# Performance work log

Measured on AMD Instinct MI355X. Metric: run time of the kernel, lower is better.

## Reference

```python
import jax, jax.numpy as jnp
import numpy as np

N = 10000
E = 256000
MUL = 32            # multiplicity per l (hidden_sizes = [32]*4)
NB = 10             # nbasis_funcs
RMAX = 3.5          # max_radius
NAVG = 25.6         # navg_neighbors
NGRAPH = 16         # number of graphs in batch
SLICES = [(0, 1), (1, 4), (4, 9), (9, 16)]  # l=0..3 blocks of the 16-dim SH rep


def _sph_harm(u):
    """Real spherical harmonics l=0..3, component normalization, on unit vectors. [E,16]"""
    x, y, z = u[:, 0], u[:, 1], u[:, 2]
    one = jnp.ones_like(x)
    s3 = 3.0 ** 0.5
    s15 = 15.0 ** 0.5
    s5 = 5.0 ** 0.5
    a = (35.0 / 8.0) ** 0.5
    b = 105.0 ** 0.5
    c = (21.0 / 8.0) ** 0.5
    d = 7.0 ** 0.5 / 2.0
    cols = [
        one,
        s3 * x, s3 * y, s3 * z,
        s15 * x * y, s15 * y * z, 0.5 * s5 * (3 * z * z - 1), s15 * x * z, 0.5 * s15 * (x * x - y * y),
        a * y * (3 * x * x - y * y), b * x * y * z, c * y * (5 * z * z - 1), d * z * (5 * z * z - 3),
        c * x * (5 * z * z - 1), 0.5 * b * z * (x * x - y * y), a * x * (x * x - 3 * y * y),
    ]
    return jnp.stack(cols, axis=1)


def _radial(emb, W1, W2):
    # FullyConnectedNet-style MLP with fan-in normalization and silu
    h = jax.nn.silu(emb @ W1 / (NB ** 0.5))
    return h @ W2 / (W1.shape[1] ** 0.5)


def _edge_geometry(pos, edge_src, edge_dst):
    vec = pos[edge_src] - pos[edge_dst]          # [E,3]
    r = jnp.linalg.norm(vec, axis=1)             # [E]
    u = vec / (r[:, None] + 1e-9)
    sh = _sph_harm(u)                            # [E,16]
    t = jnp.clip(r / RMAX, 0.0, 1.0)
    cutoff = jnp.where(r < RMAX, 0.5 * (jnp.cos(jnp.pi * t) + 1.0), 0.0)
    edge_attr = cutoff[:, None] * sh             # [E,16]
    centers = jnp.linspace(0.0, RMAX, NB)
    step = RMAX / (NB - 1)
    emb = jnp.exp(-(((r[:, None] - centers) / step) ** 2)) / 1.12 * (NB ** 0.5)
    return edge_attr, emb


def _layer(feat, edge_src, edge_dst, edge_attr, emb, Wsc, Wr1, Wr2):
    """Gated interaction block: self-connection + per-edge radial-weighted TP conv + gate."""
    n = feat.shape[0]
    # self-connection: per-l channel mixing
    sc = jnp.concatenate(
        [jnp.einsum('nci,co->noi', feat[:, :, a:b], Wsc[l]) for l, (a, b) in enumerate(SLICES)],
        axis=2) / (MUL ** 0.5)
    # per-edge weights from radial MLP: [E, 2 paths, 4 l's, MUL]
    w = _radial(emb, Wr1, Wr2).reshape(-1, 2, 4, MUL)
    xs = feat[edge_src]                          # [E,MUL,16] gather
    # path A (0e x Yl -> l) for l=0, plus path B (l x Yl -> 0e) for l=1..3 -> scalar slot
    scal = w[:, 0, 0, :] * xs[:, :, 0] * edge_attr[:, 0:1]
    parts = []
    for l, (a, b) in enumerate(SLICES):
        if l == 0:
            continue
        scal = scal + w[:, 1, l, :] * jnp.einsum('eci,ei->ec', xs[:, :, a:b], edge_attr[:, a:b])
        parts.append(w[:, 0, l, :, None] * xs[:, :, 0:1] * edge_attr[:, None, a:b])
    msg = jnp.concatenate([scal[:, :, None]] + parts, axis=2)   # [E,MUL,16]
    agg = jax.ops.segment_sum(msg, edge_dst, num_segments=n) / (NAVG ** 0.5)
    y = sc + agg
    # equivariant gate: silu on scalars, sigmoid(scalar) gates l>0 features
    s = y[:, :, 0]
    return jnp.concatenate(
        [jax.nn.silu(s)[:, :, None], y[:, :, 1:] * jax.nn.sigmoid(s)[:, :, None]], axis=2)


def _forward(pos, x, batch, edge_src, edge_dst, W_sc, Wr1, Wr2, Wf1, Wf2):
    n = pos.shape[0]
    edge_attr, emb = _edge_geometry(pos, edge_src, edge_dst)
    # lift scalar input features into the full l=0..3 layout
    feat = jnp.zeros((n, MUL, 16), x.dtype).at[:, :, 0].set(x)
    for i in range(3):
        feat = _layer(feat, edge_src, edge_dst, edge_attr, emb, W_sc[i], Wr1[i], Wr2[i])
    # final interaction block -> 1x0e output per node
    wf = _radial(emb, Wf1, Wf2).reshape(-1, 4, MUL)             # [E,4,MUL]
    xs = feat[edge_src]
    ms = wf[:, 0, :] * xs[:, :, 0] * edge_attr[:, 0:1]
    for l, (a, b) in enumerate(SLICES):
        if l == 0:
            continue
        ms = ms + wf[:, l, :] * jnp.einsum('eci,ei->ec', xs[:, :, a:b], edge_attr[:, a:b])
    node = jax.ops.segment_sum(ms.sum(axis=1) / (MUL ** 0.5), edge_dst, num_segments=n) / (NAVG ** 0.5)
    out = jax.ops.segment_sum(node, batch, num_segments=NGRAPH) / (NAVG ** 0.5)
    return out.flatten()


def setup_inputs() -> dict:
    key = jax.random.key(0)
    ks = jax.random.split(key, 10)
    pos = jax.random.uniform(ks[0], (N, 3), jnp.float32) * 5.0
    x = jax.random.normal(ks[1], (N, MUL), jnp.float32)
    batch = jnp.sort(jax.random.randint(ks[2], (N,), 0, NGRAPH, jnp.int32))
    edge_src = jax.random.randint(ks[3], (E,), 0, N, jnp.int32)
    edge_dst = jax.random.randint(ks[4], (E,), 0, N, jnp.int32)
    W_sc = jax.random.normal(ks[5], (3, 4, MUL, MUL), jnp.float32)
    Wr1 = jax.random.normal(ks[6], (3, NB, 64), jnp.float32)
    Wr2 = jax.random.normal(ks[7], (3, 64, 2 * 4 * MUL), jnp.float32)
    Wf1 = jax.random.normal(ks[8], (NB, 64), jnp.float32)
    Wf2 = jax.random.normal(ks[9], (64, 4 * MUL), jnp.float32)
    return {"pos": pos, "x": x, "batch": batch, "edge_src": edge_src, "edge_dst": edge_dst,
            "W_sc": W_sc, "Wr1": Wr1, "Wr2": Wr2, "Wf1": Wf1, "Wf2": Wf2}


def reference(pos, x, batch, edge_src, edge_dst, W_sc, Wr1, Wr2, Wf1, Wf2):
    return _forward(pos, x, batch, edge_src, edge_dst, W_sc, Wr1, Wr2, Wf1, Wf2)
```

## Files before the change

kernel.cpp:

```cpp
#include <hip/hip_runtime.h>
#include <math.h>

#define NN 10000
#define EE 256000
#define NGR 16
#define ECAP 150016

#define RSQRT10F   0.31622776601683794f
#define EMB_SCALE  2.8234621965789103f
#define INV_SQRT_MUL  0.17677669529663687f
#define INV_SQRT_NAVG 0.19764235376052372f
#define SCREC      (0.125f * INV_SQRT_NAVG)
#define STEPF      0.3888888888888889f
#define INV_STEPF  2.5714285714285716f
#define PIF        3.14159265358979323846f

__device__ __forceinline__ float sigm(float x) {
    return 1.0f / (1.0f + __expf(-x));
}

__device__ __forceinline__ void atomAddF(float* p, float v) {
    __hip_atomic_fetch_add(p, v, __ATOMIC_RELAXED, __HIP_MEMORY_SCOPE_AGENT);
}

__global__ __launch_bounds__(256) void count_kernel(
    const float* __restrict__ pos, const int* __restrict__ esrc,
    const int* __restrict__ edst, int* __restrict__ deg)
{
    int e = blockIdx.x * 256 + threadIdx.x;
    if (e >= EE) return;
    int s = esrc[e], d = edst[e];
    float vx = pos[3*s+0] - pos[3*d+0];
    float vy = pos[3*s+1] - pos[3*d+1];
    float vz = pos[3*s+2] - pos[3*d+2];
    float r2 = vx*vx + vy*vy + vz*vz;
    if (r2 < 12.25f) atomicAdd(&deg[d], 1);
}

__global__ __launch_bounds__(256) void scan_kernel(
    const int* __restrict__ deg, int* __restrict__ off, int* __restrict__ cursor)
{
    __shared__ int sbuf[256];
    const int t = threadIdx.x;
    const int start = t * 40;
    const int end = (start + 40 < NN) ? start + 40 : NN;
    int s = 0;
    for (int i = start; i < end; ++i) s += deg[i];
    sbuf[t] = s;
    __syncthreads();
    for (int d = 1; d < 256; d <<= 1) {
        int v = (t >= d) ? sbuf[t - d] : 0;
        __syncthreads();
        sbuf[t] += v;
        __syncthreads();
    }
    int run = sbuf[t] - s;
    for (int i = start; i < end; ++i) {
        off[i] = run; cursor[i] = run; run += deg[i];
    }
    if (t == 255) off[NN] = sbuf[255];
}

__global__ __launch_bounds__(256) void w1t_kernel(
    const float* __restrict__ Wr1, const float* __restrict__ Wf1,
    float* __restrict__ w1t)
{
    int t = blockIdx.x * 256 + threadIdx.x;
    if (t >= 4096) return;
    int i = t & 15;
    int j = (t >> 4) & 63;
    int l = t >> 10;
    float v;
    if (l < 3) v = (i < 10) ? Wr1[l * 640 + i * 64 + j] : 0.0f;
    else       v = (i < 10) ? Wf1[i * 64 + j] : 0.0f;
    w1t[l * 1024 + j * 16 + i] = v;
}

__global__ __launch_bounds__(256) void pack_kernel(
    const float* __restrict__ Wr2, const float* __restrict__ Wf2,
    float* __restrict__ wr2p, float* __restrict__ wf2p)
{
    const int offs[7] = {0, 32, 64, 96, 160, 192, 224};
    int t = blockIdx.x * 256 + threadIdx.x;
    if (t < 49152) {
        int k = t & 63;
        int j = (t >> 6) & 63;
        int g = (t >> 12) & 3;
        int layer = t >> 14;
        float v = 0.0f;
        if (k < 56)
            v = Wr2[layer * 16384 + j * 256 + offs[k >> 3] + g * 8 + (k & 7)];
        wr2p[t] = v;
    } else if (t < 49152 + 8192) {
        int t2 = t - 49152;
        int k = t2 & 31;
        int j = (t2 >> 5) & 63;
        int g = t2 >> 11;
        wf2p[t2] = Wf2[j * 128 + (k >> 3) * 32 + g * 8 + (k & 7)];
    }
}

__global__ __launch_bounds__(256) void scatter_kernel(
    const float* __restrict__ pos, const int* __restrict__ esrc,
    const int* __restrict__ edst, int* __restrict__ cursor,
    int* __restrict__ csrc, int* __restrict__ cdst,
    float* __restrict__ attr_soa, float* __restrict__ attr_e,
    float* __restrict__ emb_soa)
{
    int e = blockIdx.x * 256 + threadIdx.x;
    if (e >= EE) return;
    int s = esrc[e], d = edst[e];
    float vx = pos[3*s+0] - pos[3*d+0];
    float vy = pos[3*s+1] - pos[3*d+1];
    float vz = pos[3*s+2] - pos[3*d+2];
    float r2 = vx*vx + vy*vy + vz*vz;
    if (r2 >= 12.25f) return;
    float r = sqrtf(r2);
    int slot = atomicAdd(&cursor[d], 1);
    if (slot >= ECAP) return;

    float inv = 1.0f / (r + 1e-9f);
    float x = vx * inv, y = vy * inv, z = vz * inv;

    float t = r * (1.0f / 3.5f);
    float cw = 0.5f * (cosf(PIF * t) + 1.0f);

    const float s3  = 1.7320508075688772f;
    const float s15 = 3.872983346207417f;
    const float s5  = 2.23606797749979f;
    const float a4  = 2.0916500663351889f;
    const float b4  = 10.246950765959598f;
    const float c4  = 1.6201851746019651f;
    const float d4  = 1.3228756555322954f;
    float xx = x*x, yy = y*y, zz = z*z;
    float sh[16];
    sh[0]  = 1.0f;
    sh[1]  = s3 * x;
    sh[2]  = s3 * y;
    sh[3]  = s3 * z;
    sh[4]  = s15 * x * y;
    sh[5]  = s15 * y * z;
    sh[6]  = 0.5f * s5 * (3.0f*zz - 1.0f);
    sh[7]  = s15 * x * z;
    sh[8]  = 0.5f * s15 * (xx - yy);
    sh[9]  = a4 * y * (3.0f*xx - yy);
    sh[10] = b4 * x * y * z;
    sh[11] = c4 * y * (5.0f*zz - 1.0f);
    sh[12] = d4 * z * (5.0f*zz - 3.0f);
    sh[13] = c4 * x * (5.0f*zz - 1.0f);
    sh[14] = 0.5f * b4 * z * (xx - yy);
    sh[15] = a4 * x * (xx - 3.0f*yy);

    float4* ae = (float4*)(attr_e + (size_t)slot * 16);
    #pragma unroll
    for (int q = 0; q < 4; ++q)
        ae[q] = make_float4(cw*sh[q*4], cw*sh[q*4+1], cw*sh[q*4+2], cw*sh[q*4+3]);

    #pragma unroll
    for (int i = 0; i < 16; ++i)
        attr_soa[(size_t)i * ECAP + slot] = cw * sh[i];
    #pragma unroll
    for (int k = 0; k < 10; ++k) {
        float dd = (r - (float)k * STEPF) * INV_STEPF;
        emb_soa[(size_t)k * ECAP + slot] = __expf(-dd * dd) * EMB_SCALE;
    }
    csrc[slot] = s;
    cdst[slot] = d;
}

__global__ __launch_bounds__(256) void init_feat_kernel(
    const float* __restrict__ x, float* __restrict__ feat)
{
    int t = blockIdx.x * 256 + threadIdx.x;
    if (t >= NN * 512) return;
    int i = t & 15;
    int c = (t >> 4) & 31;
    int n = t >> 9;
    feat[t] = (i == 0) ? x[n * 32 + c] : 0.0f;
}

__global__ __launch_bounds__(256) void h_kernel(
    const float* __restrict__ w1t, const float* __restrict__ emb_soa,
    float* __restrict__ h_soa, const int* __restrict__ cntp)
{
    const int tid = threadIdx.x;
    int cnt = *cntp; if (cnt > ECAP) cnt = ECAP;
    if (cnt == 0) return;
    const int e = blockIdx.x * 256 + tid;
    if (blockIdx.x * 256 >= cnt) return;
    const bool alive = (e < cnt);
    const int ee = alive ? e : (cnt - 1);

    float emb[10];
    #pragma unroll
    for (int i = 0; i < 10; ++i)
        emb[i] = emb_soa[(size_t)i * ECAP + ee];

    #pragma unroll 4
    for (int j = 0; j < 64; ++j) {
        const float* wj = w1t + j * 16;
        float a = 0.0f;
        #pragma unroll
        for (int i = 0; i < 10; ++i)
            a += emb[i] * wj[i];
        a *= RSQRT10F;
        if (alive)
            h_soa[(size_t)j * ECAP + e] = a * sigm(a);
    }
}

__global__ __launch_bounds__(256, 4) void edge_mlp_kernel(
    const float* __restrict__ wr2p, const float* __restrict__ h_soa,
    const float* __restrict__ fin, float* __restrict__ rec,
    const int* __restrict__ csrc,
    const float* __restrict__ attr_soa, const int* __restrict__ cntp)
{
    const int tid = threadIdx.x;
    const int g = blockIdx.y;
    const int c0 = g * 8;
    int cnt = *cntp; if (cnt > ECAP) cnt = ECAP;
    if (cnt == 0) return;
    const int e = blockIdx.x * 256 + tid;
    if (blockIdx.x * 256 >= cnt) return;
    const bool alive = (e < cnt);
    const int ee = alive ? e : (cnt - 1);

    float attr[16];
    #pragma unroll
    for (int i = 0; i < 16; ++i)
        attr[i] = attr_soa[(size_t)i * ECAP + ee];

    const float* xb = fin + (size_t)csrc[ee] * 512;
    const float* hp = h_soa + ee;
    const float* wg = wr2p + (size_t)g * 4096;
    float4* rec4 = (float4*)rec;

    float a0[8], a1[8], a2[8], a3[8], a4[8], a5[8], a6[8];
    #pragma unroll
    for (int u = 0; u < 8; ++u) {
        a0[u] = 0.f; a1[u] = 0.f; a2[u] = 0.f; a3[u] = 0.f;
        a4[u] = 0.f; a5[u] = 0.f; a6[u] = 0.f;
    }
    #pragma unroll 4
    for (int j = 0; j < 64; ++j) {
        const float hj = hp[(size_t)j * ECAP];
        const float* w = wg + j * 64;
        #pragma unroll
        for (int u = 0; u < 8; ++u) {
            a0[u] += hj * w[u];
            a1[u] += hj * w[8 + u];
            a2[u] += hj * w[16 + u];
            a3[u] += hj * w[24 + u];
            a4[u] += hj * w[32 + u];
            a5[u] += hj * w[40 + u];
            a6[u] += hj * w[48 + u];
        }
    }
    #pragma unroll
    for (int u = 0; u < 8; ++u) {
        const int c = c0 + u;
        const float4* xv = (const float4*)(xb + c * 16);
        float4 x0 = xv[0], x1 = xv[1], x2 = xv[2], x3 = xv[3];
        float d1 = x0.y*attr[1] + x0.z*attr[2] + x0.w*attr[3];
        float d2 = x1.x*attr[4] + x1.y*attr[5] + x1.z*attr[6]
                 + x1.w*attr[7] + x2.x*attr[8];
        float d3 = x2.y*attr[9] + x2.z*attr[10] + x2.w*attr[11]
                 + x3.x*attr[12] + x3.y*attr[13] + x3.z*attr[14]
                 + x3.w*attr[15];
        const float xs0 = x0.x;
        float scal = SCREC * (a0[u]*xs0*attr[0] + a4[u]*d1 + a5[u]*d2 + a6[u]*d3);
        float px = SCREC * xs0;
        if (alive)
            rec4[(size_t)c * ECAP + e] =
                make_float4(scal, a1[u] * px, a2[u] * px, a3[u] * px);
    }
}

__global__ __launch_bounds__(256) void agg_kernel(
    const float* __restrict__ fin, float* __restrict__ fout,
    const float* __restrict__ Wsc, const float* __restrict__ rec,
    const float* __restrict__ attr_e, const int* __restrict__ off)
{
    int t = blockIdx.x * 256 + threadIdx.x;
    int c = t & 31;
    int n = t >> 5;
    if (n >= NN) return;

    float acc[16];
    #pragma unroll
    for (int i = 0; i < 16; ++i) acc[i] = 0.0f;

    const float* f = fin + (size_t)n * 512;
    for (int cin = 0; cin < 32; ++cin) {
        float w0 = Wsc[          cin * 32 + c];
        float w1 = Wsc[1024 + cin * 32 + c];
        float w2 = Wsc[2048 + cin * 32 + c];
        float w3 = Wsc[3072 + cin * 32 + c];
        const float4* fv = (const float4*)(f + cin * 16);
        float4 f0 = fv[0], f1 = fv[1], f2 = fv[2], f3 = fv[3];
        acc[0]  += f0.x * w0;
        acc[1]  += f0.y * w1; acc[2]  += f0.z * w1; acc[3]  += f0.w * w1;
        acc[4]  += f1.x * w2; acc[5]  += f1.y * w2; acc[6]  += f1.z * w2;
        acc[7]  += f1.w * w2; acc[8]  += f2.x * w2;
        acc[9]  += f2.y * w3; acc[10] += f2.z * w3; acc[11] += f2.w * w3;
        acc[12] += f3.x * w3; acc[13] += f3.y * w3; acc[14] += f3.z * w3;
        acc[15] += f3.w * w3;
    }
    #pragma unroll
    for (int i = 0; i < 16; ++i) acc[i] *= INV_SQRT_MUL;

    const float4* rec4 = (const float4*)rec;
    int e0 = off[n], e1 = off[n + 1];
    if (e1 > ECAP) e1 = ECAP;
    for (int e = e0; e < e1; ++e) {
        float4 v = rec4[(size_t)c * ECAP + e];
        const float4* av = (const float4*)(attr_e + (size_t)e * 16);
        float4 A0 = av[0], A1 = av[1], A2 = av[2], A3 = av[3];
        acc[0]  += v.x;
        acc[1]  += v.y * A0.y;
        acc[2]  += v.y * A0.z;
        acc[3]  += v.y * A0.w;
        acc[4]  += v.z * A1.x;
        acc[5]  += v.z * A1.y;
        acc[6]  += v.z * A1.z;
        acc[7]  += v.z * A1.w;
        acc[8]  += v.z * A2.x;
        acc[9]  += v.w * A2.y;
        acc[10] += v.w * A2.z;
        acc[11] += v.w * A2.w;
        acc[12] += v.w * A3.x;
        acc[13] += v.w * A3.y;
        acc[14] += v.w * A3.z;
        acc[15] += v.w * A3.w;
    }

    float s = acc[0];
    float g = sigm(s);
    float4 o0 = make_float4(s * g,      acc[1] * g,  acc[2] * g,  acc[3] * g);
    float4 o1 = make_float4(acc[4] * g, acc[5] * g,  acc[6] * g,  acc[7] * g);
    float4 o2 = make_float4(acc[8] * g, acc[9] * g,  acc[10] * g, acc[11] * g);
    float4 o3 = make_float4(acc[12] * g, acc[13] * g, acc[14] * g, acc[15] * g);
    float4* ov = (float4*)(fout + (size_t)n * 512 + c * 16);
    ov[0] = o0; ov[1] = o1; ov[2] = o2; ov[3] = o3;
}

__global__ __launch_bounds__(256, 4) void final_edge_kernel(
    const float* __restrict__ wf2p, const float* __restrict__ h_soa,
    const float* __restrict__ fin, float* __restrict__ node,
    const int* __restrict__ csrc, const int* __restrict__ cdst,
    const float* __restrict__ attr_soa, const int* __restrict__ cntp)
{
    const int tid = threadIdx.x;
    const int g = blockIdx.y;
    const int c0 = g * 8;
    int cnt = *cntp; if (cnt > ECAP) cnt = ECAP;
    if (cnt == 0) return;
    const int e = blockIdx.x * 256 + tid;
    if (blockIdx.x * 256 >= cnt) return;
    const bool alive = (e < cnt);
    const int ee = alive ? e : (cnt - 1);

    float attr[16];
    #pragma unroll
    for (int i = 0; i < 16; ++i)
        attr[i] = attr_soa[(size_t)i * ECAP + ee];

    const float* xb = fin + (size_t)csrc[ee] * 512;
    const float* hp = h_soa + ee;
    const float* wg = wf2p + (size_t)g * 2048;

    float a0[8], a1[8], a2[8], a3[8];
    #pragma unroll
    for (int u = 0; u < 8; ++u) { a0[u]=0.f; a1[u]=0.f; a2[u]=0.f; a3[u]=0.f; }
    #pragma unroll 4
    for (int j = 0; j < 64; ++j) {
        const float hj = hp[(size_t)j * ECAP];
        const float* w = wg + j * 32;
        #pragma unroll
        for (int u = 0; u < 8; ++u) {
            a0[u] += hj * w[u];
            a1[u] += hj * w[8 + u];
            a2[u] += hj * w[16 + u];
            a3[u] += hj * w[24 + u];
        }
    }
    float msum = 0.0f;
    #pragma unroll
    for (int u = 0; u < 8; ++u) {
        const int c = c0 + u;
        const float4* xv = (const float4*)(xb + c * 16);
        float4 x0 = xv[0], x1 = xv[1], x2 = xv[2], x3 = xv[3];
        float d1 = x0.y*attr[1] + x0.z*attr[2] + x0.w*attr[3];
        float d2 = x1.x*attr[4] + x1.y*attr[5] + x1.z*attr[6]
                 + x1.w*attr[7] + x2.x*attr[8];
        float d3 = x2.y*attr[9] + x2.z*attr[10] + x2.w*attr[11]
                 + x3.x*attr[12] + x3.y*attr[13] + x3.z*attr[14]
                 + x3.w*attr[15];
        msum += 0.125f * (a0[u]*x0.x*attr[0] + a1[u]*d1 + a2[u]*d2 + a3[u]*d3);
    }
    if (alive)
        atomAddF(node + cdst[ee], msum * (INV_SQRT_MUL * INV_SQRT_NAVG));
}

__global__ __launch_bounds__(256) void out_kernel(
    const float* __restrict__ node, const int* __restrict__ batch,
    float* __restrict__ out)
{
    __shared__ float bins[NGR];
    int t = blockIdx.x * 256 + threadIdx.x;
    if (threadIdx.x < NGR) bins[threadIdx.x] = 0.0f;
    __syncthreads();
    if (t < NN) atomicAdd(&bins[batch[t]], node[t] * INV_SQRT_NAVG);
    __syncthreads();
    if (threadIdx.x < NGR) atomAddF(out + threadIdx.x, bins[threadIdx.x]);
}

extern "C" void kernel_launch(void* const* d_in, const int* in_sizes, int n_in,
                              void* d_out, int out_size, void* d_ws, size_t ws_size,
                              hipStream_t stream)
{
    const float* pos  = (const float*)d_in[0];
    const float* x    = (const float*)d_in[1];
    const int*   batch= (const int*)  d_in[2];
    const int*   esrc = (const int*)  d_in[3];
    const int*   edst = (const int*)  d_in[4];
    const float* W_sc = (const float*)d_in[5];
    const float* Wr1  = (const float*)d_in[6];
    const float* Wr2  = (const float*)d_in[7];
    const float* Wf1  = (const float*)d_in[8];
    const float* Wf2  = (const float*)d_in[9];
    float* out = (float*)d_out;

    char* ws = (char*)d_ws;
    size_t off_b = 0;
    auto alloc = [&](size_t bytes) -> void* {
        void* p = ws + off_b;
        off_b = (off_b + bytes + 255) & ~(size_t)255;
        return p;
    };
    int*   deg      = (int*)  alloc((size_t)NN * 4);
    int*   off      = (int*)  alloc((size_t)(NN + 1) * 4);
    int*   cursor   = (int*)  alloc((size_t)NN * 4);
    float* node     = (float*)alloc((size_t)NN * 4);
    int*   csrc     = (int*)  alloc((size_t)ECAP * 4);
    int*   cdst     = (int*)  alloc((size_t)ECAP * 4);
    float* w1t      = (float*)alloc((size_t)4 * 1024 * 4);
    float* wr2p     = (float*)alloc((size_t)3 * 16384 * 4);
    float* wf2p     = (float*)alloc((size_t)8192 * 4);
    float* emb_soa  = (float*)alloc((size_t)10 * ECAP * 4);
    float* attr_soa = (float*)alloc((size_t)16 * ECAP * 4);
    float* attr_e   = (float*)alloc((size_t)16 * ECAP * 4);
    float* h_soa    = (float*)alloc((size_t)64 * ECAP * 4);
    float* rec      = (float*)alloc((size_t)128 * ECAP * 4);
    float* feat_a   = (float*)alloc((size_t)NN * 512 * 4);
    float* feat_b   = (float*)alloc((size_t)NN * 512 * 4);

    hipMemsetAsync(deg, 0, (size_t)NN * 4, stream);
    hipMemsetAsync(node, 0, (size_t)NN * 4, stream);
    hipMemsetAsync(d_out, 0, (size_t)out_size * 4, stream);

    count_kernel<<<(EE + 255) / 256, 256, 0, stream>>>(pos, esrc, edst, deg);
    scan_kernel<<<1, 256, 0, stream>>>(deg, off, cursor);
    w1t_kernel<<<16, 256, 0, stream>>>(Wr1, Wf1, w1t);
    pack_kernel<<<(49152 + 8192 + 255) / 256, 256, 0, stream>>>(
        Wr2, Wf2, wr2p, wf2p);
    scatter_kernel<<<(EE + 255) / 256, 256, 0, stream>>>(
        pos, esrc, edst, cursor, csrc, cdst, attr_soa, attr_e, emb_soa);
    init_feat_kernel<<<(NN * 512 + 255) / 256, 256, 0, stream>>>(x, feat_a);

    const int* cntp = off + NN;
    float* fin = feat_a;
    float* fout = feat_b;
    dim3 egrid(ECAP / 256, 4);
    for (int layer = 0; layer < 3; ++layer) {
        h_kernel<<<ECAP / 256, 256, 0, stream>>>(
            w1t + layer * 1024, emb_soa, h_soa, cntp);
        edge_mlp_kernel<<<egrid, 256, 0, stream>>>(
            wr2p + (size_t)layer * 16384, h_soa, fin, rec,
            csrc, attr_soa, cntp);
        agg_kernel<<<(NN * 32 + 255) / 256, 256, 0, stream>>>(
            fin, fout, W_sc + layer * 4096, rec, attr_e, off);
        float* tmp = fin; fin = fout; fout = tmp;
    }
    h_kernel<<<ECAP / 256, 256, 0, stream>>>(
        w1t + 3 * 1024, emb_soa, h_soa, cntp);
    final_edge_kernel<<<egrid, 256, 0, stream>>>(
        wf2p, h_soa, fin, node, csrc, cdst, attr_soa, cntp);
    out_kernel<<<(NN + 255) / 256, 256, 0, stream>>>(node, batch, out);
}
```

Baseline: 875.3 us.

## Reorder final edge contraction and replace node atomics with CSR segmented reduction

The final edge kernel now computes per-edge angular dot products first, then contracts them with the packed Wf2 weights inside the hidden-unit loop. This avoids keeping 32 per-channel accumulators and uses 2 channel groups of 16 instead of 4 groups of 8, repacking Wf2 to match. Per-edge partial sums are written to a buffer instead of being atomically added to node entries. The output kernel then reduces each node's CSR edge range directly, which removes the node array, its memset and the global atomics. The trade-off is that each edge now does more arithmetic per hidden unit, and the output kernel runs serial per-node loops whose lengths vary.

```diff
diff --git a/kernel.cpp b/kernel.cpp
--- a/kernel.cpp
+++ b/kernel.cpp
@@ -93,10 +93,11 @@
         wr2p[t] = v;
     } else if (t < 49152 + 8192) {
         int t2 = t - 49152;
-        int k = t2 & 31;
-        int j = (t2 >> 5) & 63;
-        int g = t2 >> 11;
-        wf2p[t2] = Wf2[j * 128 + (k >> 3) * 32 + g * 8 + (k & 7)];
+        int u = t2 & 15;
+        int l = (t2 >> 4) & 3;
+        int j = (t2 >> 6) & 63;
+        int g = t2 >> 12;
+        wf2p[t2] = Wf2[j * 128 + l * 32 + g * 16 + u];
     }
 }
 
@@ -346,13 +347,13 @@
 
 __global__ __launch_bounds__(256, 4) void final_edge_kernel(
     const float* __restrict__ wf2p, const float* __restrict__ h_soa,
-    const float* __restrict__ fin, float* __restrict__ node,
-    const int* __restrict__ csrc, const int* __restrict__ cdst,
+    const float* __restrict__ fin, float* __restrict__ fbuf,
+    const int* __restrict__ csrc,
     const float* __restrict__ attr_soa, const int* __restrict__ cntp)
 {
     const int tid = threadIdx.x;
     const int g = blockIdx.y;
-    const int c0 = g * 8;
+    const int c0 = g * 16;
     int cnt = *cntp; if (cnt > ECAP) cnt = ECAP;
     if (cnt == 0) return;
     const int e = blockIdx.x * 256 + tid;
@@ -366,51 +367,58 @@
         attr[i] = attr_soa[(size_t)i * ECAP + ee];
 
     const float* xb = fin + (size_t)csrc[ee] * 512;
+    float d0[16], d1[16], d2[16], d3[16];
+    #pragma unroll
+    for (int u = 0; u < 16; ++u) {
+        const float4* xv = (const float4*)(xb + (c0 + u) * 16);
+        float4 x0 = xv[0], x1 = xv[1], x2 = xv[2], x3 = xv[3];
+        d0[u] = x0.x * attr[0];
+        d1[u] = x0.y*attr[1] + x0.z*attr[2] + x0.w*attr[3];
+        d2[u] = x1.x*attr[4] + x1.y*attr[5] + x1.z*attr[6]
+              + x1.w*attr[7] + x2.x*attr[8];
+        d3[u] = x2.y*attr[9] + x2.z*attr[10] + x2.w*attr[11]
+              + x3.x*attr[12] + x3.y*attr[13] + x3.z*attr[14]
+              + x3.w*attr[15];
+    }
+
     const float* hp = h_soa + ee;
-    const float* wg = wf2p + (size_t)g * 2048;
-
-    float a0[8], a1[8], a2[8], a3[8];
-    #pragma unroll
-    for (int u = 0; u < 8; ++u) { a0[u]=0.f; a1[u]=0.f; a2[u]=0.f; a3[u]=0.f; }
-    #pragma unroll 4
+    const float* wg = wf2p + (size_t)g * 4096;
+    float acc0 = 0.f, acc1 = 0.f, acc2 = 0.f, acc3 = 0.f;
+    #pragma unroll 2
     for (int j = 0; j < 64; ++j) {
         const float hj = hp[(size_t)j * ECAP];
-        const float* w = wg + j * 32;
+        const float* w = wg + j * 64;
+        float t0 = 0.f, t1 = 0.f, t2 = 0.f, t3 = 0.f;
         #pragma unroll
-        for (int u = 0; u < 8; ++u) {
-            a0[u] += hj * w[u];
-            a1[u] += hj * w[8 + u];
-            a2[u] += hj * w[16 + u];
-            a3[u] += hj * w[24 + u];
+        for (int u = 0; u < 16; ++u) {
+            t0 += d0[u] * w[u];
+            t1 += d1[u] * w[16 + u];
+            t2 += d2[u] * w[32 + u];
+            t3 += d3[u] * w[48 + u];
         }
-    }
-    float msum = 0.0f;
-    #pragma unroll
-    for (int u = 0; u < 8; ++u) {
-        const int c = c0 + u;
-        const float4* xv = (const float4*)(xb + c * 16);
-        float4 x0 = xv[0], x1 = xv[1], x2 = xv[2], x3 = xv[3];
-        float d1 = x0.y*attr[1] + x0.z*attr[2] + x0.w*attr[3];
-        float d2 = x1.x*attr[4] + x1.y*attr[5] + x1.z*attr[6]
-                 + x1.w*attr[7] + x2.x*attr[8];
-        float d3 = x2.y*attr[9] + x2.z*attr[10] + x2.w*attr[11]
-                 + x3.x*attr[12] + x3.y*attr[13] + x3.z*attr[14]
-                 + x3.w*attr[15];
-        msum += 0.125f * (a0[u]*x0.x*attr[0] + a1[u]*d1 + a2[u]*d2 + a3[u]*d3);
+        acc0 += hj * t0; acc1 += hj * t1;
+        acc2 += hj * t2; acc3 += hj * t3;
     }
     if (alive)
-        atomAddF(node + cdst[ee], msum * (INV_SQRT_MUL * INV_SQRT_NAVG));
+        fbuf[(size_t)g * ECAP + e] = (acc0 + acc1 + acc2 + acc3) * 0.125f;
 }
 
 __global__ __launch_bounds__(256) void out_kernel(
-    const float* __restrict__ node, const int* __restrict__ batch,
-    float* __restrict__ out)
+    const float* __restrict__ fbuf, const int* __restrict__ off,
+    const int* __restrict__ batch, float* __restrict__ out)
 {
     __shared__ float bins[NGR];
     int t = blockIdx.x * 256 + threadIdx.x;
     if (threadIdx.x < NGR) bins[threadIdx.x] = 0.0f;
     __syncthreads();
-    if (t < NN) atomicAdd(&bins[batch[t]], node[t] * INV_SQRT_NAVG);
+    if (t < NN) {
+        int e0 = off[t], e1 = off[t + 1];
+        if (e1 > ECAP) e1 = ECAP;
+        float s = 0.0f;
+        for (int e = e0; e < e1; ++e)
+            s += fbuf[e] + fbuf[(size_t)ECAP + e];
+        atomicAdd(&bins[batch[t]], s * (INV_SQRT_MUL * (1.0f / 25.6f)));
+    }
     __syncthreads();
     if (threadIdx.x < NGR) atomAddF(out + threadIdx.x, bins[threadIdx.x]);
 }
@@ -441,7 +449,6 @@
     int*   deg      = (int*)  alloc((size_t)NN * 4);
     int*   off      = (int*)  alloc((size_t)(NN + 1) * 4);
     int*   cursor   = (int*)  alloc((size_t)NN * 4);
-    float* node     = (float*)alloc((size_t)NN * 4);
     int*   csrc     = (int*)  alloc((size_t)ECAP * 4);
     int*   cdst     = (int*)  alloc((size_t)ECAP * 4);
     float* w1t      = (float*)alloc((size_t)4 * 1024 * 4);
@@ -456,7 +463,6 @@
     float* feat_b   = (float*)alloc((size_t)NN * 512 * 4);
 
     hipMemsetAsync(deg, 0, (size_t)NN * 4, stream);
-    hipMemsetAsync(node, 0, (size_t)NN * 4, stream);
     hipMemsetAsync(d_out, 0, (size_t)out_size * 4, stream);
 
     count_kernel<<<(EE + 255) / 256, 256, 0, stream>>>(pos, esrc, edst, deg);
@@ -484,7 +490,8 @@
     }
     h_kernel<<<ECAP / 256, 256, 0, stream>>>(
         w1t + 3 * 1024, emb_soa, h_soa, cntp);
-    final_edge_kernel<<<egrid, 256, 0, stream>>>(
-        wf2p, h_soa, fin, node, csrc, cdst, attr_soa, cntp);
-    out_kernel<<<(NN + 255) / 256, 256, 0, stream>>>(node, batch, out);
-}
+    float* fbuf = rec;
+    final_edge_kernel<<<dim3(ECAP / 256, 2), 256, 0, stream>>>(
+        wf2p, h_soa, fin, fbuf, csrc, attr_soa, cntp);
+    out_kernel<<<(NN + 255) / 256, 256, 0, stream>>>(fbuf, off, batch, out);
+}
```

Result: no change. 879.6 us (+0.5%).
